# Kernel optimization log

Hardware: AMD Instinct MI355X
Metric: run time of the kernel (lower is better)

## Reference

```python
import jax, jax.numpy as jnp
import numpy as np

B, C, H, W = 32, 512, 32, 32
INNER = C // 8


def setup_inputs() -> dict:
    key = jax.random.key(0)
    k_x, k_f, k_g, k_h = jax.random.split(key, 4)
    x = jax.random.normal(k_x, (B, C, H, W), dtype=jnp.float32)
    # 1x1 Conv1d weights (bias=False) are plain [out, in] matrices.
    s_in = 1.0 / np.sqrt(C)
    Wf = jax.random.uniform(k_f, (INNER, C), dtype=jnp.float32, minval=-s_in, maxval=s_in)
    Wg = jax.random.uniform(k_g, (INNER, C), dtype=jnp.float32, minval=-s_in, maxval=s_in)
    Wh = jax.random.uniform(k_h, (C, C), dtype=jnp.float32, minval=-s_in, maxval=s_in)
    return {"x": x, "Wf": Wf, "Wg": Wg, "Wh": Wh}


def reference(x, Wf, Wg, Wh):
    b, c = x.shape[0], x.shape[1]
    xf = x.reshape(b, c, -1)                       # [B, C, N]
    f = jnp.einsum('ic,bcn->bin', Wf, xf)          # [B, inner, N]
    g = jnp.einsum('ic,bcn->bin', Wg, xf)          # [B, inner, N]
    h = jnp.einsum('oc,bcn->bon', Wh, xf)          # [B, C, N]
    sim = jnp.einsum('bin,bim->bnm', f, g)         # f^T g -> [B, N, N]
    beta = jax.nn.softmax(sim, axis=1)             # softmax over the f-index axis (dim=1)
    o = jnp.einsum('bcn,bnm->bcm', h, beta)        # [B, C, N]
    return o
```

## Files before the change

kernel.cpp:

```cpp
#include <hip/hip_runtime.h>
#include <stdint.h>

#define CDIM 512
#define NPIX 1024
#define IDIM 64

#define WS_BATCH (65536 + 65536 + 524288)
#define XT_OFF   ((size_t)32 * WS_BATCH)
#define XT_ELEMS ((size_t)32 * 1024 * 512)
#define WH_OFF   (XT_OFF + XT_ELEMS)
#define P_OFF    XT_OFF
#define P_ELEMS  ((size_t)32 * 1024 * 1024)
#define LP_OFF   (P_OFF + P_ELEMS)

typedef __bf16 bf16x8 __attribute__((ext_vector_type(8)));
typedef _Float16 f16x8 __attribute__((ext_vector_type(8)));
typedef float f32x4 __attribute__((ext_vector_type(4)));

__device__ __forceinline__ unsigned short f2bf(float f) {
    union { float f; uint32_t u; } v; v.f = f;
    uint32_t u = v.u;
    u += 0x7fffu + ((u >> 16) & 1u);
    return (unsigned short)(u >> 16);
}

__device__ __forceinline__ f32x4 mfma_bf(bf16x8 a, bf16x8 b, f32x4 c) {
    return __builtin_amdgcn_mfma_f32_16x16x32_bf16(a, b, c, 0, 0, 0);
}
__device__ __forceinline__ f32x4 mfma_h(f16x8 a, f16x8 b, f32x4 c) {
    return __builtin_amdgcn_mfma_f32_16x16x32_f16(a, b, c, 0, 0, 0);
}
__device__ __forceinline__ void gld_lds16(const void* g, void* l) {
    __builtin_amdgcn_global_load_lds(
        (const __attribute__((address_space(1))) unsigned int*)g,
        (__attribute__((address_space(3))) unsigned int*)l,
        16, 0, 0);
}
__device__ __forceinline__ void barrier_mem() {
    asm volatile("" ::: "memory");
    __builtin_amdgcn_s_barrier();
    asm volatile("" ::: "memory");
}
__device__ __forceinline__ int swz(int by) { return by ^ (((by >> 7) & 3) << 4); }

__global__ __launch_bounds__(256) void wcvt(
    const float* __restrict__ Wf, const float* __restrict__ Wg,
    const float* __restrict__ Wh, _Float16* __restrict__ wh)
{
    int e = (blockIdx.x * 256 + threadIdx.x) * 4;
    int r = e >> 9, k = e & 511;
    const float* src;
    if (r < 64)       src = Wf + (size_t)r * 512 + k;
    else if (r < 128) src = Wg + (size_t)(r - 64) * 512 + k;
    else              src = Wh + (size_t)(r - 128) * 512 + k;
    float4 v = *(const float4*)src;
    _Float16 h4[4] = {(_Float16)v.x, (_Float16)v.y, (_Float16)v.z, (_Float16)v.w};
    *(ushort4*)(wh + e) = *(ushort4*)h4;
}

__global__ __launch_bounds__(256) void xcvt(
    const float* __restrict__ x, _Float16* __restrict__ xT)
{
    __shared__ _Float16 tile[64][72];
    const int b = blockIdx.z, c0 = blockIdx.y * 64, n0 = blockIdx.x * 64;
    const int t = threadIdx.x;
    const float* xb = x + ((size_t)b * CDIM + c0) * NPIX + n0;
    #pragma unroll
    for (int p = 0; p < 4; ++p) {
        int ci = p * 16 + (t >> 4);
        int nj = (t & 15) * 4;
        float4 v = *(const float4*)(xb + (size_t)ci * NPIX + nj);
        tile[nj + 0][ci] = (_Float16)v.x;
        tile[nj + 1][ci] = (_Float16)v.y;
        tile[nj + 2][ci] = (_Float16)v.z;
        tile[nj + 3][ci] = (_Float16)v.w;
    }
    __syncthreads();
    _Float16* dst = xT + ((size_t)b * NPIX + n0) * CDIM + c0;
    #pragma unroll
    for (int p = 0; p < 2; ++p) {
        int n  = p * 32 + (t >> 3);
        int cc = (t & 7) * 8;
        ushort4 a  = *(ushort4*)&tile[n][cc];
        ushort4 bq = *(ushort4*)&tile[n][cc + 4];
        *(ushort4*)(dst + (size_t)n * CDIM + cc)     = a;
        *(ushort4*)(dst + (size_t)n * CDIM + cc + 4) = bq;
    }
}

__global__ __launch_bounds__(256, 4) void fgh_mfma(
    const _Float16* __restrict__ wh, const _Float16* __restrict__ xT,
    unsigned short* __restrict__ ws)
{
    const int orig = blockIdx.x;
    const int work = (orig & 7) * 160 + (orig >> 3);
    const int b    = work / 40;
    const int tile = work % 40;
    const int tr = tile >> 3, tn = tile & 7;

    const int t = threadIdx.x, lane = t & 63, w = t >> 6;
    const int lr = lane & 15, lg = lane >> 4;
    const int wr = w >> 1, wc = w & 1;

    __shared__ _Float16 Abuf[2][128 * 32];
    __shared__ _Float16 Bbuf[2][128 * 32];

    const _Float16* Ag = wh + (size_t)(tr * 128) * CDIM;
    const _Float16* Bg = xT + ((size_t)b * NPIX + tn * 128) * CDIM;

    int offA[4], offB[4];
    #pragma unroll
    for (int mf = 0; mf < 4; ++mf)
        offA[mf] = swz((wr * 64 + mf * 16 + lr) * 64 + lg * 16);
    #pragma unroll
    for (int nf = 0; nf < 4; ++nf)
        offB[nf] = swz((wc * 64 + nf * 16 + lr) * 64 + lg * 16);

    f32x4 acc[4][4];
    #pragma unroll
    for (int i = 0; i < 4; ++i)
        #pragma unroll
        for (int j = 0; j < 4; ++j) acc[i][j] = (f32x4){0.f, 0.f, 0.f, 0.f};

    auto stage = [&](int buf, int k0) {
        #pragma unroll
        for (int p = 0; p < 2; ++p) {
            int q = p * 256 + t;
            gld_lds16(Ag + (size_t)(q >> 2) * CDIM + k0 + ((q & 3) ^ ((q >> 3) & 3)) * 8,
                      (char*)&Abuf[buf][0] + q * 16);
        }
        #pragma unroll
        for (int p = 0; p < 2; ++p) {
            int q = p * 256 + t;
            gld_lds16(Bg + (size_t)(q >> 2) * CDIM + k0 + ((q & 3) ^ ((q >> 3) & 3)) * 8,
                      (char*)&Bbuf[buf][0] + q * 16);
        }
    };

    stage(0, 0);
    stage(1, 32);

    #pragma unroll 1
    for (int ks = 0; ks < 16; ++ks) {
        const int cur = ks & 1;
        if (ks < 15) asm volatile("s_waitcnt vmcnt(4)" ::: "memory");
        else         asm volatile("s_waitcnt vmcnt(0)" ::: "memory");
        barrier_mem();

        const char* Ab = (const char*)&Abuf[cur][0];
        const char* Bb = (const char*)&Bbuf[cur][0];
        f16x8 af[4];
        #pragma unroll
        for (int mf = 0; mf < 4; ++mf)
            af[mf] = *(const f16x8*)(Ab + offA[mf]);
        #pragma unroll
        for (int nf = 0; nf < 4; ++nf) {
            f16x8 bv = *(const f16x8*)(Bb + offB[nf]);
            #pragma unroll
            for (int mf = 0; mf < 4; ++mf)
                acc[mf][nf] = mfma_h(af[mf], bv, acc[mf][nf]);
        }

        barrier_mem();
        if (ks + 2 < 16) stage(cur, (ks + 2) * 32);
    }

    unsigned short* base = ws + (size_t)b * WS_BATCH;
    const int nbase = tn * 128 + wc * 64;
    if (tr == 0) {
        unsigned short* dst = base + (wr ? 65536 : 0);
        #pragma unroll
        for (int mf = 0; mf < 4; ++mf) {
            const int i0 = mf * 16 + lg * 4;
            #pragma unroll
            for (int nf = 0; nf < 4; ++nf) {
                int n = nbase + nf * 16 + lr;
                ushort4 v;
                v.x = f2bf(acc[mf][nf][0]); v.y = f2bf(acc[mf][nf][1]);
                v.z = f2bf(acc[mf][nf][2]); v.w = f2bf(acc[mf][nf][3]);
                *(ushort4*)(dst + (size_t)n * 64 + i0) = v;
            }
        }
    } else {
        unsigned short* hd = base + 131072;
        const int cbase = (tr - 1) * 128 + wr * 64;
        #pragma unroll
        for (int mf = 0; mf < 4; ++mf)
            #pragma unroll
            for (int nf = 0; nf < 4; ++nf) {
                int n = nbase + nf * 16 + lr;
                #pragma unroll
                for (int j = 0; j < 4; ++j) {
                    int c = cbase + mf * 16 + lg * 4 + j;
                    hd[(size_t)c * NPIX + n] = f2bf(acc[mf][nf][j]);
                }
            }
    }
}

__global__ __launch_bounds__(256, 3) void attn_sm(
    const unsigned short* __restrict__ ws, unsigned short* __restrict__ P,
    float* __restrict__ Lp)
{
    const int orig = blockIdx.x;
    const int work = (orig & 7) * 256 + (orig >> 3);
    const int b    = work >> 6;
    const int tile = work & 63;
    const int mt = tile >> 2, nt = tile & 3;
    const int m0 = mt * 64, n0 = nt * 256;

    const int t = threadIdx.x, lane = t & 63, w = t >> 6;
    const int lr = lane & 15, lg = lane >> 4;

    const unsigned short* fT = ws + (size_t)b * WS_BATCH;
    const unsigned short* gT = fT + 65536;

    __shared__ unsigned short Ab[2][64 * 32];
    __shared__ unsigned short Bb[2][256 * 32];
    __shared__ float red[4][64];
    __shared__ unsigned short rp[4][16][72];

    #pragma unroll
    for (int kc = 0; kc < 2; ++kc) {
        {
            int q = t;
            gld_lds16(gT + (size_t)(m0 + (q >> 2)) * 64 + kc * 32 + ((q & 3) ^ ((q >> 3) & 3)) * 8,
                      (char*)&Ab[kc][0] + q * 16);
        }
        #pragma unroll
        for (int p = 0; p < 4; ++p) {
            int q = p * 256 + t;
            gld_lds16(fT + (size_t)(n0 + (q >> 2)) * 64 + kc * 32 + ((q & 3) ^ ((q >> 3) & 3)) * 8,
                      (char*)&Bb[kc][0] + q * 16);
        }
    }
    __syncthreads();

    int offA[4], offB[4];
    #pragma unroll
    for (int mf = 0; mf < 4; ++mf)
        offA[mf] = swz((mf * 16 + lr) * 64 + lg * 16);
    #pragma unroll
    for (int nf = 0; nf < 4; ++nf)
        offB[nf] = swz((w * 64 + nf * 16 + lr) * 64 + lg * 16);

    f32x4 acc[4][4];
    #pragma unroll
    for (int i = 0; i < 4; ++i)
        #pragma unroll
        for (int j = 0; j < 4; ++j) acc[i][j] = (f32x4){0.f, 0.f, 0.f, 0.f};

    #pragma unroll
    for (int kc = 0; kc < 2; ++kc) {
        const char* Abc = (const char*)&Ab[kc][0];
        const char* Bbc = (const char*)&Bb[kc][0];
        bf16x8 af[4];
        #pragma unroll
        for (int mf = 0; mf < 4; ++mf)
            af[mf] = *(const bf16x8*)(Abc + offA[mf]);
        #pragma unroll
        for (int nf = 0; nf < 4; ++nf) {
            bf16x8 bv = *(const bf16x8*)(Bbc + offB[nf]);
            #pragma unroll
            for (int mf = 0; mf < 4; ++mf)
                acc[mf][nf] = mfma_bf(af[mf], bv, acc[mf][nf]);
        }
    }

    #pragma unroll
    for (int mf = 0; mf < 4; ++mf) {
        #pragma unroll
        for (int j = 0; j < 4; ++j) {
            float s = 0.f;
            #pragma unroll
            for (int nf = 0; nf < 4; ++nf) {
                float e = __expf(acc[mf][nf][j]);
                acc[mf][nf][j] = e;
                s += e;
            }
            s += __shfl_xor(s, 1);
            s += __shfl_xor(s, 2);
            s += __shfl_xor(s, 4);
            s += __shfl_xor(s, 8);
            if (lr == 0) red[w][mf * 16 + lg * 4 + j] = s;
        }
    }
    __syncthreads();
    if (t < 64) {
        float s = red[0][t] + red[1][t] + red[2][t] + red[3][t];
        Lp[(size_t)nt * 32768 + (size_t)b * 1024 + m0 + t] = s;
    }

    unsigned short* Pb = P + (size_t)b * NPIX * NPIX;
    #pragma unroll
    for (int mf = 0; mf < 4; ++mf) {
        #pragma unroll
        for (int nf = 0; nf < 4; ++nf)
            #pragma unroll
            for (int j = 0; j < 4; ++j)
                rp[w][lg * 4 + j][nf * 16 + lr] = f2bf(acc[mf][nf][j]);
        #pragma unroll
        for (int ii = 0; ii < 2; ++ii) {
            int row = ii * 8 + (lane >> 3);
            int ch  = lane & 7;
            ushort4 v0 = *(ushort4*)&rp[w][row][ch * 8];
            ushort4 v1 = *(ushort4*)&rp[w][row][ch * 8 + 4];
            unsigned short* dst = Pb + (size_t)(m0 + mf * 16 + row) * NPIX
                                     + n0 + w * 64 + ch * 8;
            *(ushort4*)(dst)     = v0;
            *(ushort4*)(dst + 4) = v1;
        }
    }
}

__global__ __launch_bounds__(512, 2) void attn_pv(
    const unsigned short* __restrict__ P, const unsigned short* __restrict__ ws,
    const float* __restrict__ Lp, float* __restrict__ out)
{
    const int orig = blockIdx.x;
    const int work = (orig & 7) * 32 + (orig >> 3);
    const int b    = work >> 3;
    const int tile = work & 7;
    const int m0   = (tile >> 1) * 256;
    const int c0   = (tile & 1) * 256;

    const int t = threadIdx.x, lane = t & 63, w = t >> 6;
    const int lr = lane & 15, lg = lane >> 4;
    const int wr = w >> 2, wc = w & 3;

    __shared__ __align__(16) char smem[131072];

    const unsigned short* Ag = P + ((size_t)b * NPIX + m0) * NPIX;
    const unsigned short* Bg = ws + (size_t)b * WS_BATCH + 131072 + (size_t)c0 * NPIX;

    const int sk0 = ((lg) ^ (lr & 7)) * 16;
    const int sk1 = ((4 + lg) ^ (lr & 7)) * 16;
    const int rAbase = (wr * 128 + lr) * 128;
    const int rBbase = (wc * 64 + lr) * 128;

    f32x4 acc[8][4];
    #pragma unroll
    for (int i = 0; i < 8; ++i)
        #pragma unroll
        for (int j = 0; j < 4; ++j) acc[i][j] = (f32x4){0.f, 0.f, 0.f, 0.f};

    auto stage_half = [&](int buf, int isB, int half, int kt) {
        const unsigned short* G = isB ? Bg : Ag;
        char* L = smem + isB * 65536 + buf * 32768 + half * 16384;
        #pragma unroll
        for (int l = 0; l < 2; ++l) {
            int q = l * 512 + t;
            gld_lds16(G + (size_t)(half * 128 + (q >> 3)) * NPIX + kt * 64
                        + (((q & 7) ^ ((q >> 3) & 7)) * 8),
                      L + q * 16);
        }
    };

    stage_half(0, 0, 0, 0); stage_half(0, 0, 1, 0);
    stage_half(0, 1, 0, 0); stage_half(0, 1, 1, 0);
    stage_half(1, 1, 0, 1); stage_half(1, 1, 1, 1);
    asm volatile("s_waitcnt vmcnt(4)" ::: "memory");
    barrier_mem();

    bf16x8 bfr[4][2];

    #pragma unroll 1
    for (int j = 0; j < 8; ++j) {
        const bool nl = (j < 7);
        #pragma unroll
        for (int grp = 0; grp < 2; ++grp) {
            const char* Abase = smem + grp * 32768;
            const char* Bbase = smem + 65536 + grp * 32768;
            #pragma unroll
            for (int p = 0; p < 4; ++p) {
                if (p == 0) {
                    #pragma unroll
                    for (int nf = 0; nf < 4; ++nf) {
                        bfr[nf][0] = *(const bf16x8*)(Bbase + rBbase + nf * 2048 + sk0);
                        bfr[nf][1] = *(const bf16x8*)(Bbase + rBbase + nf * 2048 + sk1);
                    }
                }
                bf16x8 af[2][2];
                #pragma unroll
                for (int e = 0; e < 2; ++e) {
                    af[e][0] = *(const bf16x8*)(Abase + rAbase + (p * 2 + e) * 2048 + sk0);
                    af[e][1] = *(const bf16x8*)(Abase + rAbase + (p * 2 + e) * 2048 + sk1);
                }
                if (grp == 0) {
                    if (p == 0) stage_half(1, 0, 0, 2 * j + 1);
                    if (p == 1) stage_half(1, 0, 1, 2 * j + 1);
                    if (p == 2 && nl) stage_half(0, 1, 0, 2 * j + 2);
                    if (p == 3 && nl) stage_half(0, 1, 1, 2 * j + 2);
                } else {
                    if (p == 0 && nl) stage_half(0, 0, 0, 2 * j + 2);
                    if (p == 1 && nl) stage_half(0, 0, 1, 2 * j + 2);
                    if (p == 2 && nl) stage_half(1, 1, 0, 2 * j + 3);
                    if (p == 3 && nl) stage_half(1, 1, 1, 2 * j + 3);
                }
                if (p == 3) {
                    if (nl) asm volatile("s_waitcnt vmcnt(4)" ::: "memory");
                    else    asm volatile("s_waitcnt vmcnt(0)" ::: "memory");
                }
                barrier_mem();
                __builtin_amdgcn_s_setprio(1);
                #pragma unroll
                for (int ks = 0; ks < 2; ++ks)
                    #pragma unroll
                    for (int e = 0; e < 2; ++e)
                        #pragma unroll
                        for (int nf = 0; nf < 4; ++nf)
                            acc[p * 2 + e][nf] =
                                mfma_bf(af[e][ks], bfr[nf][ks], acc[p * 2 + e][nf]);
                __builtin_amdgcn_s_setprio(0);
            }
        }
    }

    #pragma unroll
    for (int mf = 0; mf < 8; ++mf) {
        const size_t mi = (size_t)b * 1024 + m0 + wr * 128 + mf * 16 + lg * 4;
        f32x4 L = *(const f32x4*)&Lp[mi]
                + *(const f32x4*)&Lp[32768 + mi]
                + *(const f32x4*)&Lp[65536 + mi]
                + *(const f32x4*)&Lp[98304 + mi];
        f32x4 rinv;
        #pragma unroll
        for (int j = 0; j < 4; ++j) rinv[j] = 1.0f / L[j];
        #pragma unroll
        for (int nf = 0; nf < 4; ++nf) {
            f32x4 o = acc[mf][nf] * rinv;
            int c = c0 + wc * 64 + nf * 16 + lr;
            int m = m0 + wr * 128 + mf * 16 + lg * 4;
            *(f32x4*)(out + ((size_t)b * CDIM + c) * NPIX + m) = o;
        }
    }
}

extern "C" void kernel_launch(void* const* d_in, const int* in_sizes, int n_in,
                              void* d_out, int out_size, void* d_ws, size_t ws_size,
                              hipStream_t stream) {
    const float* x  = (const float*)d_in[0];
    const float* Wf = (const float*)d_in[1];
    const float* Wg = (const float*)d_in[2];
    const float* Wh = (const float*)d_in[3];
    unsigned short* ws = (unsigned short*)d_ws;
    _Float16* xT = (_Float16*)(ws + XT_OFF);
    _Float16* wh = (_Float16*)(ws + WH_OFF);
    unsigned short* P = ws + P_OFF;
    float* Lp = (float*)(ws + LP_OFF);
    float* out = (float*)d_out;

    wcvt<<<320, 256, 0, stream>>>(Wf, Wg, Wh, wh);
    xcvt<<<dim3(16, 8, 32), 256, 0, stream>>>(x, xT);
    fgh_mfma<<<1280, 256, 0, stream>>>(wh, xT, ws);
    attn_sm<<<2048, 256, 0, stream>>>(ws, P, Lp);
    attn_pv<<<256, 512, 0, stream>>>(P, ws, Lp, out);
}
```

Measured before the change: 119.5 us.

## Split fused f/g/h projection GEMM into f/g kernel and large-tile h kernel

The combined projection kernel is split in two. f/g are now computed by a 128-wide-tile kernel over the first 128 weight rows. h goes to a new 512-thread kernel with 256x256 tiles, K steps of 64, a double-buffered async LDS pipeline with XOR swizzle and interleaved staging, and raised wave priority around the MFMAs. Larger tiles are meant to increase operand reuse and cut global traffic for the dominant h GEMM. The cost is an extra launch, 128KB of LDS per block and only 256 blocks for h, which lowers occupancy.

```diff
diff --git a/kernel.cpp b/kernel.cpp
--- a/kernel.cpp
+++ b/kernel.cpp
@@ -88,15 +88,14 @@
     }
 }
 
-__global__ __launch_bounds__(256, 4) void fgh_mfma(
+__global__ __launch_bounds__(256, 4) void fg_mfma(
     const _Float16* __restrict__ wh, const _Float16* __restrict__ xT,
     unsigned short* __restrict__ ws)
 {
     const int orig = blockIdx.x;
-    const int work = (orig & 7) * 160 + (orig >> 3);
-    const int b    = work / 40;
-    const int tile = work % 40;
-    const int tr = tile >> 3, tn = tile & 7;
+    const int work = (orig & 7) * 32 + (orig >> 3);
+    const int b    = work >> 3;
+    const int tn   = work & 7;
 
     const int t = threadIdx.x, lane = t & 63, w = t >> 6;
     const int lr = lane & 15, lg = lane >> 4;
@@ -105,7 +104,7 @@
     __shared__ _Float16 Abuf[2][128 * 32];
     __shared__ _Float16 Bbuf[2][128 * 32];
 
-    const _Float16* Ag = wh + (size_t)(tr * 128) * CDIM;
+    const _Float16* Ag = wh;
     const _Float16* Bg = xT + ((size_t)b * NPIX + tn * 128) * CDIM;
 
     int offA[4], offB[4];
@@ -167,35 +166,136 @@
 
     unsigned short* base = ws + (size_t)b * WS_BATCH;
     const int nbase = tn * 128 + wc * 64;
-    if (tr == 0) {
-        unsigned short* dst = base + (wr ? 65536 : 0);
-        #pragma unroll
-        for (int mf = 0; mf < 4; ++mf) {
-            const int i0 = mf * 16 + lg * 4;
-            #pragma unroll
-            for (int nf = 0; nf < 4; ++nf) {
-                int n = nbase + nf * 16 + lr;
-                ushort4 v;
-                v.x = f2bf(acc[mf][nf][0]); v.y = f2bf(acc[mf][nf][1]);
-                v.z = f2bf(acc[mf][nf][2]); v.w = f2bf(acc[mf][nf][3]);
-                *(ushort4*)(dst + (size_t)n * 64 + i0) = v;
+    unsigned short* dst = base + (wr ? 65536 : 0);
+    #pragma unroll
+    for (int mf = 0; mf < 4; ++mf) {
+        const int i0 = mf * 16 + lg * 4;
+        #pragma unroll
+        for (int nf = 0; nf < 4; ++nf) {
+            int n = nbase + nf * 16 + lr;
+            ushort4 v;
+            v.x = f2bf(acc[mf][nf][0]); v.y = f2bf(acc[mf][nf][1]);
+            v.z = f2bf(acc[mf][nf][2]); v.w = f2bf(acc[mf][nf][3]);
+            *(ushort4*)(dst + (size_t)n * 64 + i0) = v;
+        }
+    }
+}
+
+__global__ __launch_bounds__(512, 2) void h_mfma(
+    const _Float16* __restrict__ wh, const _Float16* __restrict__ xT,
+    unsigned short* __restrict__ ws)
+{
+    const int orig = blockIdx.x;
+    const int work = (orig & 7) * 32 + (orig >> 3);
+    const int b    = work >> 3;
+    const int tile = work & 7;
+    const int m0   = (tile >> 2) * 256;
+    const int n0   = (tile & 3) * 256;
+
+    const int t = threadIdx.x, lane = t & 63, w = t >> 6;
+    const int lr = lane & 15, lg = lane >> 4;
+    const int wr = w >> 2, wc = w & 3;
+
+    __shared__ __align__(16) char smem[131072];
+
+    const _Float16* Ag = wh + (size_t)(128 + m0) * CDIM;
+    const _Float16* Bg = xT + ((size_t)b * NPIX + n0) * CDIM;
+
+    const int sk0 = ((lg) ^ (lr & 7)) * 16;
+    const int sk1 = ((4 + lg) ^ (lr & 7)) * 16;
+    const int rAbase = (wr * 128 + lr) * 128;
+    const int rBbase = (wc * 64 + lr) * 128;
+
+    f32x4 acc[8][4];
+    #pragma unroll
+    for (int i = 0; i < 8; ++i)
+        #pragma unroll
+        for (int j = 0; j < 4; ++j) acc[i][j] = (f32x4){0.f, 0.f, 0.f, 0.f};
+
+    auto stage_half = [&](int buf, int isB, int half, int kt) {
+        const _Float16* G = isB ? Bg : Ag;
+        char* L = smem + isB * 65536 + buf * 32768 + half * 16384;
+        #pragma unroll
+        for (int l = 0; l < 2; ++l) {
+            int q = l * 512 + t;
+            gld_lds16(G + (size_t)(half * 128 + (q >> 3)) * CDIM + kt * 64
+                        + (((q & 7) ^ ((q >> 3) & 7)) * 8),
+                      L + q * 16);
+        }
+    };
+
+    stage_half(0, 0, 0, 0); stage_half(0, 0, 1, 0);
+    stage_half(0, 1, 0, 0); stage_half(0, 1, 1, 0);
+    stage_half(1, 1, 0, 1); stage_half(1, 1, 1, 1);
+    asm volatile("s_waitcnt vmcnt(4)" ::: "memory");
+    barrier_mem();
+
+    f16x8 bfr[4][2];
+
+    #pragma unroll 1
+    for (int j = 0; j < 4; ++j) {
+        const bool nl = (j < 3);
+        #pragma unroll
+        for (int grp = 0; grp < 2; ++grp) {
+            const char* Abase = smem + grp * 32768;
+            const char* Bbase = smem + 65536 + grp * 32768;
+            #pragma unroll
+            for (int p = 0; p < 4; ++p) {
+                if (p == 0) {
+                    #pragma unroll
+                    for (int nf = 0; nf < 4; ++nf) {
+                        bfr[nf][0] = *(const f16x8*)(Bbase + rBbase + nf * 2048 + sk0);
+                        bfr[nf][1] = *(const f16x8*)(Bbase + rBbase + nf * 2048 + sk1);
+                    }
+                }
+                f16x8 af[2][2];
+                #pragma unroll
+                for (int e = 0; e < 2; ++e) {
+                    af[e][0] = *(const f16x8*)(Abase + rAbase + (p * 2 + e) * 2048 + sk0);
+                    af[e][1] = *(const f16x8*)(Abase + rAbase + (p * 2 + e) * 2048 + sk1);
+                }
+                if (grp == 0) {
+                    if (p == 0) stage_half(1, 0, 0, 2 * j + 1);
+                    if (p == 1) stage_half(1, 0, 1, 2 * j + 1);
+                    if (p == 2 && nl) stage_half(0, 1, 0, 2 * j + 2);
+                    if (p == 3 && nl) stage_half(0, 1, 1, 2 * j + 2);
+                } else {
+                    if (p == 0 && nl) stage_half(0, 0, 0, 2 * j + 2);
+                    if (p == 1 && nl) stage_half(0, 0, 1, 2 * j + 2);
+                    if (p == 2 && nl) stage_half(1, 1, 0, 2 * j + 3);
+                    if (p == 3 && nl) stage_half(1, 1, 1, 2 * j + 3);
+                }
+                if (p == 3) {
+                    if (nl) asm volatile("s_waitcnt vmcnt(4)" ::: "memory");
+                    else    asm volatile("s_waitcnt vmcnt(0)" ::: "memory");
+                }
+                barrier_mem();
+                __builtin_amdgcn_s_setprio(1);
+                #pragma unroll
+                for (int ks = 0; ks < 2; ++ks)
+                    #pragma unroll
+                    for (int e = 0; e < 2; ++e)
+                        #pragma unroll
+                        for (int nf = 0; nf < 4; ++nf)
+                            acc[p * 2 + e][nf] =
+                                mfma_h(af[e][ks], bfr[nf][ks], acc[p * 2 + e][nf]);
+                __builtin_amdgcn_s_setprio(0);
             }
         }
-    } else {
-        unsigned short* hd = base + 131072;
-        const int cbase = (tr - 1) * 128 + wr * 64;
-        #pragma unroll
-        for (int mf = 0; mf < 4; ++mf)
-            #pragma unroll
-            for (int nf = 0; nf < 4; ++nf) {
-                int n = nbase + nf * 16 + lr;
-                #pragma unroll
-                for (int j = 0; j < 4; ++j) {
-                    int c = cbase + mf * 16 + lg * 4 + j;
-                    hd[(size_t)c * NPIX + n] = f2bf(acc[mf][nf][j]);
-                }
+    }
+
+    unsigned short* hd = ws + (size_t)b * WS_BATCH + 131072;
+    #pragma unroll
+    for (int mf = 0; mf < 8; ++mf)
+        #pragma unroll
+        for (int nf = 0; nf < 4; ++nf) {
+            int n = n0 + wc * 64 + nf * 16 + lr;
+            #pragma unroll
+            for (int j = 0; j < 4; ++j) {
+                int c = m0 + wr * 128 + mf * 16 + lg * 4 + j;
+                hd[(size_t)c * NPIX + n] = f2bf(acc[mf][nf][j]);
             }
-    }
+        }
 }
 
 __global__ __launch_bounds__(256, 3) void attn_sm(
@@ -452,7 +552,8 @@
 
     wcvt<<<320, 256, 0, stream>>>(Wf, Wg, Wh, wh);
     xcvt<<<dim3(16, 8, 32), 256, 0, stream>>>(x, xT);
-    fgh_mfma<<<1280, 256, 0, stream>>>(wh, xT, ws);
+    fg_mfma<<<256, 256, 0, stream>>>(wh, xT, ws);
+    h_mfma<<<256, 512, 0, stream>>>(wh, xT, ws);
     attn_sm<<<2048, 256, 0, stream>>>(ws, P, Lp);
     attn_pv<<<256, 512, 0, stream>>>(P, ws, Lp, out);
 }
```

After: 121.3 us. About the same (+1.6%).

## Merge conversion kernels and stage h epilogue through LDS for coalesced stores

Applied to the files above, without the earlier changes.

Merges the weight-conversion and x-transpose kernels into one launch by adding an extra grid slice for the weight blocks, which removes one kernel launch. The fgh_mfma epilogue for the h output now writes bf16 results into a per-wave padded LDS tile and then stores 16-byte vectors per lane. Before, each element was written as a scattered 2-byte global store. Shared memory grows to 36 KB per block to hold the staging tile, which may reduce occupancy at 4 blocks per CU.

```diff
diff --git a/kernel.cpp b/kernel.cpp
--- a/kernel.cpp
+++ b/kernel.cpp
@@ -16,6 +16,7 @@
 typedef __bf16 bf16x8 __attribute__((ext_vector_type(8)));
 typedef _Float16 f16x8 __attribute__((ext_vector_type(8)));
 typedef float f32x4 __attribute__((ext_vector_type(4)));
+typedef unsigned short u16x8 __attribute__((ext_vector_type(8)));
 
 __device__ __forceinline__ unsigned short f2bf(float f) {
     union { float f; uint32_t u; } v; v.f = f;
@@ -43,27 +44,29 @@
 }
 __device__ __forceinline__ int swz(int by) { return by ^ (((by >> 7) & 3) << 4); }
 
-__global__ __launch_bounds__(256) void wcvt(
+__global__ __launch_bounds__(256) void xw_cvt(
+    const float* __restrict__ x,
     const float* __restrict__ Wf, const float* __restrict__ Wg,
-    const float* __restrict__ Wh, _Float16* __restrict__ wh)
+    const float* __restrict__ Wh,
+    _Float16* __restrict__ xT, _Float16* __restrict__ wh)
 {
-    int e = (blockIdx.x * 256 + threadIdx.x) * 4;
-    int r = e >> 9, k = e & 511;
-    const float* src;
-    if (r < 64)       src = Wf + (size_t)r * 512 + k;
-    else if (r < 128) src = Wg + (size_t)(r - 64) * 512 + k;
-    else              src = Wh + (size_t)(r - 128) * 512 + k;
-    float4 v = *(const float4*)src;
-    _Float16 h4[4] = {(_Float16)v.x, (_Float16)v.y, (_Float16)v.z, (_Float16)v.w};
-    *(ushort4*)(wh + e) = *(ushort4*)h4;
-}
-
-__global__ __launch_bounds__(256) void xcvt(
-    const float* __restrict__ x, _Float16* __restrict__ xT)
-{
+    const int t = threadIdx.x;
+    if (blockIdx.y == 8) {
+        int wb = blockIdx.z * 16 + blockIdx.x;
+        if (wb >= 320) return;
+        int e = (wb * 256 + t) * 4;
+        int r = e >> 9, k = e & 511;
+        const float* src;
+        if (r < 64)       src = Wf + (size_t)r * 512 + k;
+        else if (r < 128) src = Wg + (size_t)(r - 64) * 512 + k;
+        else              src = Wh + (size_t)(r - 128) * 512 + k;
+        float4 v = *(const float4*)src;
+        _Float16 h4[4] = {(_Float16)v.x, (_Float16)v.y, (_Float16)v.z, (_Float16)v.w};
+        *(ushort4*)(wh + e) = *(ushort4*)h4;
+        return;
+    }
     __shared__ _Float16 tile[64][72];
     const int b = blockIdx.z, c0 = blockIdx.y * 64, n0 = blockIdx.x * 64;
-    const int t = threadIdx.x;
     const float* xb = x + ((size_t)b * CDIM + c0) * NPIX + n0;
     #pragma unroll
     for (int p = 0; p < 4; ++p) {
@@ -102,8 +105,7 @@
     const int lr = lane & 15, lg = lane >> 4;
     const int wr = w >> 1, wc = w & 1;
 
-    __shared__ _Float16 Abuf[2][128 * 32];
-    __shared__ _Float16 Bbuf[2][128 * 32];
+    __shared__ __align__(16) char smem[36864];
 
     const _Float16* Ag = wh + (size_t)(tr * 128) * CDIM;
     const _Float16* Bg = xT + ((size_t)b * NPIX + tn * 128) * CDIM;
@@ -127,13 +129,13 @@
         for (int p = 0; p < 2; ++p) {
             int q = p * 256 + t;
             gld_lds16(Ag + (size_t)(q >> 2) * CDIM + k0 + ((q & 3) ^ ((q >> 3) & 3)) * 8,
-                      (char*)&Abuf[buf][0] + q * 16);
+                      smem + buf * 8192 + q * 16);
         }
         #pragma unroll
         for (int p = 0; p < 2; ++p) {
             int q = p * 256 + t;
             gld_lds16(Bg + (size_t)(q >> 2) * CDIM + k0 + ((q & 3) ^ ((q >> 3) & 3)) * 8,
-                      (char*)&Bbuf[buf][0] + q * 16);
+                      smem + 16384 + buf * 8192 + q * 16);
         }
     };
 
@@ -147,8 +149,8 @@
         else         asm volatile("s_waitcnt vmcnt(0)" ::: "memory");
         barrier_mem();
 
-        const char* Ab = (const char*)&Abuf[cur][0];
-        const char* Bb = (const char*)&Bbuf[cur][0];
+        const char* Ab = smem + cur * 8192;
+        const char* Bb = smem + 16384 + cur * 8192;
         f16x8 af[4];
         #pragma unroll
         for (int mf = 0; mf < 4; ++mf)
@@ -182,19 +184,24 @@
             }
         }
     } else {
+        unsigned short* sc = (unsigned short*)smem + w * 4608;
+        #pragma unroll
+        for (int mf = 0; mf < 4; ++mf)
+            #pragma unroll
+            for (int nf = 0; nf < 4; ++nf)
+                #pragma unroll
+                for (int j = 0; j < 4; ++j)
+                    sc[(mf * 16 + lg * 4 + j) * 72 + nf * 16 + lr] =
+                        f2bf(acc[mf][nf][j]);
         unsigned short* hd = base + 131072;
         const int cbase = (tr - 1) * 128 + wr * 64;
         #pragma unroll
-        for (int mf = 0; mf < 4; ++mf)
-            #pragma unroll
-            for (int nf = 0; nf < 4; ++nf) {
-                int n = nbase + nf * 16 + lr;
-                #pragma unroll
-                for (int j = 0; j < 4; ++j) {
-                    int c = cbase + mf * 16 + lg * 4 + j;
-                    hd[(size_t)c * NPIX + n] = f2bf(acc[mf][nf][j]);
-                }
-            }
+        for (int ii = 0; ii < 8; ++ii) {
+            int cl = ii * 8 + (lane >> 3);
+            int nl = (lane & 7) * 8;
+            u16x8 v = *(const u16x8*)&sc[cl * 72 + nl];
+            *(u16x8*)(hd + (size_t)(cbase + cl) * NPIX + nbase + nl) = v;
+        }
     }
 }
 
@@ -450,8 +457,7 @@
     float* Lp = (float*)(ws + LP_OFF);
     float* out = (float*)d_out;
 
-    wcvt<<<320, 256, 0, stream>>>(Wf, Wg, Wh, wh);
-    xcvt<<<dim3(16, 8, 32), 256, 0, stream>>>(x, xT);
+    xw_cvt<<<dim3(16, 9, 32), 256, 0, stream>>>(x, Wf, Wg, Wh, xT, wh);
     fgh_mfma<<<1280, 256, 0, stream>>>(wh, xT, ws);
     attn_sm<<<2048, 256, 0, stream>>>(ws, P, Lp);
     attn_pv<<<256, 512, 0, stream>>>(P, ws, Lp, out);
```

Measured after the change: 113.2 us. 1.06x faster.
